# Optimization experiments

Measured on AMD Instinct MI355X. Metric: run time of the kernel, lower is better.

## Reference

```python
import jax, jax.numpy as jnp
import numpy as np

N = 10000        # nodes
E = 160000       # active edges
NS = 128         # scalar (0e) channels per tensor
NV = 64          # vector (1o) channels per tensor
LAT = 64         # latent dim
AVG_NEIGH = 16.0
SQ2 = float(np.sqrt(2.0))
SQ3 = float(np.sqrt(3.0))
EPS = 1e-5


def setup_inputs() -> dict:
    key = jax.random.key(0)
    ks = jax.random.split(key, 24)
    rn = lambda k, s: jax.random.normal(k, s, jnp.float32)
    d = {}
    d["latents"] = rn(ks[0], (E, LAT))
    d["node_features"] = rn(ks[1], (N, NS + 3 * NV))
    d["edge_features"] = rn(ks[2], (E, NS + 3 * NV))
    d["edge_sh"] = rn(ks[3], (E, 4))
    d["edge_index"] = jax.random.randint(ks[4], (2, E), 0, N)
    d["atom_type"] = jax.random.randint(ks[5], (N,), 0, 10)
    d["active_edges"] = jnp.arange(E)
    # separable layer norm affine params (node and edge)
    d["g_s_n"] = jnp.ones((NS,), jnp.float32); d["b_s_n"] = jnp.zeros((NS,), jnp.float32)
    d["g_v_n"] = jnp.ones((NV,), jnp.float32)
    d["g_s_e"] = jnp.ones((NS,), jnp.float32); d["b_s_e"] = jnp.zeros((NS,), jnp.float32)
    d["g_v_e"] = jnp.ones((NV,), jnp.float32)
    # FullyConnectedTensorProduct weights (path-normalized init).
    # tp input: 2*NS scalars, 2*NV vectors; sh: 1 scalar + 1 vector;
    # tp output: NS+NV scalars (scalars+gates), NV vectors.
    nSt, nVt, nSo = 2 * NS, 2 * NV, NS + NV
    d["W_ss0"] = rn(ks[6], (nSt, nSo)) / np.sqrt(nSt * 2)
    d["W_vv0"] = rn(ks[7], (nVt, nSo)) / np.sqrt(nVt * 2)
    d["W_sv1"] = rn(ks[8], (nSt, NV)) / np.sqrt(nSt * 3)
    d["W_vs1"] = rn(ks[9], (nVt, NV)) / np.sqrt(nVt * 3)
    d["W_vv1"] = rn(ks[10], (nVt, NV)) / np.sqrt(nVt * 3)
    # lin_post (per-l channel mixing)
    d["Wp_s"] = rn(ks[11], (NS, NS)) / np.sqrt(NS)
    d["Wp_v"] = rn(ks[12], (NV, NV)) / np.sqrt(NV)
    # env_embed_mlps: single linear latent -> weight_numel (NS+NV channels)
    d["W_env"] = rn(ks[13], (LAT, NS + NV)) / np.sqrt(LAT)
    # linear_res
    d["Wr_s"] = rn(ks[14], (NS, NS)) / np.sqrt(NS)
    d["Wr_v"] = rn(ks[15], (NV, NV)) / np.sqrt(NV)
    return d


def _sep_ln(x, g_s, b_s, g_v):
    # separable layer norm: standard LN on scalars, RMS-of-norms on vectors
    s = x[:, :NS]
    v = x[:, NS:].reshape(-1, NV, 3)
    mu = s.mean(-1, keepdims=True)
    var = ((s - mu) ** 2).mean(-1, keepdims=True)
    s = (s - mu) * jax.lax.rsqrt(var + EPS) * g_s + b_s
    vn = jnp.mean(jnp.sum(v * v, -1), -1, keepdims=True)  # (B,1)
    v = v * jax.lax.rsqrt(vn + EPS)[:, :, None] * g_v[None, :, None]
    return s, v


def _forward(latents, node_features, edge_features, edge_sh, edge_index,
             atom_type, active_edges,
             g_s_n, b_s_n, g_v_n, g_s_e, b_s_e, g_v_e,
             W_ss0, W_vv0, W_sv1, W_vs1, W_vv1,
             Wp_s, Wp_v, W_env, Wr_s, Wr_v):
    ec = edge_index[0][active_edges]                      # (E,) center nodes
    ns, nv = _sep_ln(node_features, g_s_n, b_s_n, g_v_n)
    es, ev = _sep_ln(edge_features, g_s_e, b_s_e, g_v_e)
    S = jnp.concatenate([ns[ec], es], axis=-1)            # (E, 2*NS)
    V = jnp.concatenate([nv[ec], ev], axis=1)             # (E, 2*NV, 3)
    sh0 = edge_sh[:, :1]                                  # (E,1)
    sh1 = edge_sh[:, 1:]                                  # (E,3)
    # fully-connected tensor product (tp_in x sh -> gate input)
    dotV = jnp.einsum('ecd,ed->ec', V, sh1) / SQ3         # 1x1->0
    out0 = (S * sh0) @ W_ss0 + dotV @ W_vv0               # (E, NS+NV) scalars
    out_v = (S @ W_sv1)[:, :, None] * sh1[:, None, :]     # 0x1->1
    out_v = out_v + jnp.einsum('ecd,cf->efd', V, W_vs1) * sh0[:, :, None]  # 1x0->1
    cross = jnp.cross(V, sh1[:, None, :]) / SQ2           # 1x1->1
    out_v = out_v + jnp.einsum('ecd,cf->efd', cross, W_vv1)  # (E, NV, 3)
    # gate
    s = jax.nn.silu(out0[:, :NS])
    gates = jax.nn.sigmoid(out0[:, NS:])
    v = out_v * gates[:, :, None]
    # lin_post
    s = s @ Wp_s
    v = jnp.einsum('ecd,cf->efd', v, Wp_v)
    # env weights from latents (elementwise linear per channel)
    w = latents[active_edges] @ W_env                     # (E, NS+NV)
    s = s * w[:, :NS]
    v = v * w[:, NS:][:, :, None]
    msg = jnp.concatenate([s, v.reshape(-1, 3 * NV)], axis=-1)  # (E, 320)
    agg = jax.ops.segment_sum(msg, ec, num_segments=N)
    agg = agg * jnp.float32(1.0 / np.sqrt(AVG_NEIGH))
    # residual linear on raw node features
    rs = node_features[:, :NS] @ Wr_s
    rv = jnp.einsum('ncd,cf->nfd', node_features[:, NS:].reshape(-1, NV, 3), Wr_v)
    res = jnp.concatenate([rs, rv.reshape(-1, 3 * NV)], axis=-1)
    return res + agg


def reference(latents, node_features, edge_features, edge_sh, edge_index,
              atom_type, active_edges,
              g_s_n, b_s_n, g_v_n, g_s_e, b_s_e, g_v_e,
              W_ss0, W_vv0, W_sv1, W_vs1, W_vv1,
              Wp_s, Wp_v, W_env, Wr_s, Wr_v):
    return _forward(latents, node_features, edge_features, edge_sh, edge_index,
                    atom_type, active_edges,
                    g_s_n, b_s_n, g_v_n, g_s_e, b_s_e, g_v_e,
                    W_ss0, W_vv0, W_sv1, W_vs1, W_vv1,
                    Wp_s, Wp_v, W_env, Wr_s, Wr_v)
```

## Files before the change

kernel.cpp:

```cpp
#include <hip/hip_runtime.h>

#define N_NODES 10000
#define N_EDGES 160000
#define NSC 128
#define ROW 320
#define EPS_LN 1e-5f
#define INV_SQ2 0.70710678118654752440f
#define INV_SQ3 0.57735026918962576451f

typedef unsigned short bfraw;
typedef __attribute__((ext_vector_type(8))) short short8;
typedef __attribute__((ext_vector_type(4))) float float4x;

__device__ __forceinline__ float bf2f(bfraw u) {
    union { unsigned int i; float f; } x; x.i = ((unsigned int)u) << 16; return x.f;
}
__device__ __forceinline__ bfraw f2bf(float f) {
    union { float f; unsigned int i; } x; x.f = f;
    unsigned int i = x.i;
    unsigned int lsb = (i >> 16) & 1u;
    i += 0x7fffu + lsb;
    return (bfraw)(i >> 16);
}
template<bool B> __device__ __forceinline__ float LD(const void* p, size_t i) {
    if (B) return bf2f(((const bfraw*)p)[i]);
    else   return ((const float*)p)[i];
}
template<bool B> __device__ __forceinline__ void ST(void* p, size_t i, float v) {
    if (B) ((bfraw*)p)[i] = f2bf(v);
    else   ((float*)p)[i] = v;
}
__device__ __forceinline__ float wred64(float v) {
#pragma unroll
    for (int o = 32; o > 0; o >>= 1) v += __shfl_xor(v, o, 64);
    return v;
}
__device__ __forceinline__ void wredx12(float a[12]) {
#pragma unroll
    for (int o = 32; o > 0; o >>= 1) {
        float t[12];
#pragma unroll
        for (int i = 0; i < 12; i++) t[i] = __shfl_xor(a[i], o, 64);
#pragma unroll
        for (int i = 0; i < 12; i++) a[i] += t[i];
    }
}
__device__ __forceinline__ float silu_f(float x) { return x / (1.0f + __expf(-x)); }
__device__ __forceinline__ float sigm_f(float x) { return 1.0f / (1.0f + __expf(-x)); }

#define MFMA16(a, b, c) __builtin_amdgcn_mfma_f32_16x16x32_bf16((a), (b), (c), 0, 0, 0)

__device__ __forceinline__ int SDI(int r, int c) { return r * 384 + (c ^ ((r & 7) << 3)); }
__device__ __forceinline__ int X64(int r, int c) { return r * 64  + (c ^ ((r & 7) << 3)); }
__device__ __forceinline__ int SPI(int r, int c) { return r * 128 + (c ^ ((r & 7) << 3)); }
__device__ __forceinline__ int WVI(int r, int c) { return r * 192 + (c ^ ((r & 7) << 2)); }

__global__ void detect_k(const void* g, int* flag) {
    if (threadIdx.x == 0 && blockIdx.x == 0)
        *flag = (((const unsigned int*)g)[0] == 0x3F803F80u) ? 1 : 0;
}

__global__ void pack_all_k(
    const void* Wss0, const void* Wvv0, const void* Wsv1, const void* Wvs1,
    const void* Wvv1, const void* Wps,  const void* Wpv,  const void* Wenv,
    const void* Wrs,  const void* Wrv,
    bfraw* __restrict__ dst, const int* __restrict__ flag)
{
    int idx = blockIdx.x * 256 + threadIdx.x;
    if (idx >= 159744) return;
    const void* src; int K, N, base;
    if      (idx <  49152) { src = Wss0; K = 256; N = 192; base = 0; }
    else if (idx <  73728) { src = Wvv0; K = 128; N = 192; base = 49152; }
    else if (idx <  90112) { src = Wsv1; K = 256; N =  64; base = 73728; }
    else if (idx <  98304) { src = Wvs1; K = 128; N =  64; base = 90112; }
    else if (idx < 106496) { src = Wvv1; K = 128; N =  64; base = 98304; }
    else if (idx < 122880) { src = Wps;  K = 128; N = 128; base = 106496; }
    else if (idx < 126976) { src = Wpv;  K =  64; N =  64; base = 122880; }
    else if (idx < 139264) { src = Wenv; K =  64; N = 192; base = 126976; }
    else if (idx < 155648) { src = Wrs;  K = 128; N = 128; base = 139264; }
    else                   { src = Wrv;  K =  64; N =  64; base = 155648; }
    int li = idx - base;
    int j = li & 7, l = (li >> 3) & 63, t = li >> 9;
    int NT = N >> 4;
    int nt = t % NT, kt = t / NT;
    int k = kt * 32 + ((l >> 4) << 3) + j;
    int n = (nt << 4) + (l & 15);
    float v = (*flag) ? bf2f(((const bfraw*)src)[(size_t)k * N + n])
                      : ((const float*)src)[(size_t)k * N + n];
    dst[idx] = f2bf(v);
}

__global__ void count_k(const int* __restrict__ eidx, const int* __restrict__ act,
                        int* __restrict__ counts) {
    int e = blockIdx.x * 256 + threadIdx.x;
    if (e < N_EDGES) atomicAdd(&counts[eidx[act[e]]], 1);
}

__global__ __launch_bounds__(1024) void scan_k(const int* __restrict__ counts,
                                               int* __restrict__ starts) {
    __shared__ int wsum[16];
    int t = threadIdx.x;
    int lo = t * 10;
    int lanev = t & 63, wv = t >> 6;
    int c[10];
    int s = 0;
    if (lo < N_NODES) {
#pragma unroll
        for (int j = 0; j < 10; j++) { c[j] = counts[lo + j]; s += c[j]; }
    }
    int ps = s;
#pragma unroll
    for (int o = 1; o < 64; o <<= 1) {
        int u = __shfl_up(ps, o, 64);
        if (lanev >= o) ps += u;
    }
    if (lanev == 63) wsum[wv] = ps;
    __syncthreads();
    if (t == 0) {
        int acc = 0;
#pragma unroll
        for (int i = 0; i < 16; i++) { int v = wsum[i]; wsum[i] = acc; acc += v; }
        starts[N_NODES] = acc;
    }
    __syncthreads();
    if (lo < N_NODES) {
        int acc = wsum[wv] + ps - s;
#pragma unroll
        for (int j = 0; j < 10; j++) { starts[lo + j] = acc; acc += c[j]; }
    }
}

__global__ void fill_k(const int* __restrict__ eidx, const int* __restrict__ act,
                       const int* __restrict__ starts, int* __restrict__ cursor,
                       int* __restrict__ csr) {
    int e = blockIdx.x * 256 + threadIdx.x;
    if (e < N_EDGES) {
        int n = eidx[act[e]];
        int pos = atomicAdd(&cursor[n], 1);
        csr[starts[n] + pos] = e;
    }
}

template<bool B>
__device__ __forceinline__ void node_ln_body(int n, int lane,
    const void* nf, const void* g_s, const void* b_s, const void* g_v,
    float* __restrict__ nsnv)
{
    size_t base = (size_t)n * ROW;
    float s0 = LD<B>(nf, base + lane), s1 = LD<B>(nf, base + 64 + lane);
    float mu = wred64(s0 + s1) * (1.0f / 128.0f);
    float d0 = s0 - mu, d1 = s1 - mu;
    float var = wred64(d0 * d0 + d1 * d1) * (1.0f / 128.0f);
    float rs = rsqrtf(var + EPS_LN);
    float o0 = d0 * rs * LD<B>(g_s, lane) + LD<B>(b_s, lane);
    float o1 = d1 * rs * LD<B>(g_s, 64 + lane) + LD<B>(b_s, 64 + lane);
    float vx = LD<B>(nf, base + NSC + 3 * lane);
    float vy = LD<B>(nf, base + NSC + 3 * lane + 1);
    float vz = LD<B>(nf, base + NSC + 3 * lane + 2);
    float vn = wred64(vx * vx + vy * vy + vz * vz) * (1.0f / 64.0f);
    float rv = rsqrtf(vn + EPS_LN) * LD<B>(g_v, lane);
    float* o = nsnv + base;
    o[lane] = o0; o[64 + lane] = o1;
    o[NSC + 3 * lane] = vx * rv; o[NSC + 3 * lane + 1] = vy * rv; o[NSC + 3 * lane + 2] = vz * rv;
}

__global__ __launch_bounds__(256) void node_ln_k(
    const void* nf, const void* g_s, const void* b_s, const void* g_v,
    float* __restrict__ nsnv, const int* __restrict__ flag)
{
    int w = threadIdx.x >> 6, lane = threadIdx.x & 63;
    int n = blockIdx.x * 4 + w;
    if (*flag) node_ln_body<true >(n, lane, nf, g_s, b_s, g_v, nsnv);
    else       node_ln_body<false>(n, lane, nf, g_s, b_s, g_v, nsnv);
}

template<bool B>
__device__ void edge_body(char* smem, int tid,
    const float* __restrict__ nsnv,
    const void* ef, const void* esh,
    const int* __restrict__ eidx, const int* __restrict__ act,
    const void* lat,
    const void* g_s_e, const void* b_s_e, const void* g_v_e,
    const bfraw* __restrict__ pk,
    bfraw* __restrict__ msg)
{
    bfraw* SD     = (bfraw*)(smem);
    bfraw* Vn     = (bfraw*)(smem + 12288);
    bfraw* Ve     = (bfraw*)(smem + 18432);
    bfraw* gate_u = (bfraw*)(smem + 18432);
    bfraw* sp_u   = (bfraw*)(smem + 20480);
    bfraw* lat_u  = (bfraw*)(smem + 24576);
    float* sh_f   = (float*)(smem + 26624);
    float* wenv_f = (float*)(smem);

    const bfraw* pWss0 = pk;
    const bfraw* pWvv0 = pk + 49152;
    const bfraw* pWsv1 = pk + 73728;
    const bfraw* pWvs1 = pk + 90112;
    const bfraw* pWvv1 = pk + 98304;
    const bfraw* pWps  = pk + 106496;
    const bfraw* pWpv  = pk + 122880;
    const bfraw* pWenv = pk + 126976;

    const int w = tid >> 6, lane = tid & 63;
    const int nl = lane & 15, mq = lane >> 4;
    const int e0 = blockIdx.x * 16;

    float gse0 = LD<B>(g_s_e, lane), gse1 = LD<B>(g_s_e, 64 + lane);
    float bse0 = LD<B>(b_s_e, lane), bse1 = LD<B>(b_s_e, 64 + lane);
    float gve  = LD<B>(g_v_e, lane);

    float es0[4], es1[4], ex[4], ey[4], ez[4];
    float shv[4][4];
#pragma unroll
    for (int i = 0; i < 4; i++) {
        int el = w * 4 + i, e = e0 + el;
        int ae = act[e];
        int cnv = eidx[ae];
        shv[i][0] = LD<B>(esh, (size_t)e * 4 + 0);
        shv[i][1] = LD<B>(esh, (size_t)e * 4 + 1);
        shv[i][2] = LD<B>(esh, (size_t)e * 4 + 2);
        shv[i][3] = LD<B>(esh, (size_t)e * 4 + 3);
        size_t eb = (size_t)e * ROW;
        es0[i] = LD<B>(ef, eb + lane);
        es1[i] = LD<B>(ef, eb + 64 + lane);
        ex[i]  = LD<B>(ef, eb + NSC + 3 * lane);
        ey[i]  = LD<B>(ef, eb + NSC + 3 * lane + 1);
        ez[i]  = LD<B>(ef, eb + NSC + 3 * lane + 2);
        float la = LD<B>(lat, (size_t)ae * 64 + lane);
        const float* nr = nsnv + (size_t)cnv * ROW;
        float n0 = nr[lane], n1 = nr[64 + lane];
        float nx = nr[NSC + 3 * lane], ny = nr[NSC + 3 * lane + 1], nz = nr[NSC + 3 * lane + 2];
        SD[SDI(el, lane)]       = f2bf(n0);
        SD[SDI(el, 64 + lane)]  = f2bf(n1);
        SD[SDI(el, 256 + lane)] = f2bf((nx * shv[i][1] + ny * shv[i][2] + nz * shv[i][3]) * INV_SQ3);
        Vn[X64(el, lane)]       = f2bf(nx);
        Vn[X64(16 + el, lane)]  = f2bf(ny);
        Vn[X64(32 + el, lane)]  = f2bf(nz);
        lat_u[X64(el, lane)]    = f2bf(la);
        if (lane == 0) {
            sh_f[el * 4]     = shv[i][0]; sh_f[el * 4 + 1] = shv[i][1];
            sh_f[el * 4 + 2] = shv[i][2]; sh_f[el * 4 + 3] = shv[i][3];
        }
    }
    float red[12];
#pragma unroll
    for (int i = 0; i < 4; i++) {
        red[i]     = es0[i] + es1[i];
        red[4 + i] = es0[i] * es0[i] + es1[i] * es1[i];
        red[8 + i] = ex[i] * ex[i] + ey[i] * ey[i] + ez[i] * ez[i];
    }
    wredx12(red);
#pragma unroll
    for (int i = 0; i < 4; i++) {
        int el = w * 4 + i;
        float mu  = red[i] * (1.0f / 128.0f);
        float var = red[4 + i] * (1.0f / 128.0f) - mu * mu;
        float rs  = rsqrtf(var + EPS_LN);
        float o0  = (es0[i] - mu) * rs * gse0 + bse0;
        float o1  = (es1[i] - mu) * rs * gse1 + bse1;
        float rv  = rsqrtf(red[8 + i] * (1.0f / 64.0f) + EPS_LN) * gve;
        float exn = ex[i] * rv, eyn = ey[i] * rv, ezn = ez[i] * rv;
        SD[SDI(el, 128 + lane)] = f2bf(o0);
        SD[SDI(el, 192 + lane)] = f2bf(o1);
        SD[SDI(el, 320 + lane)] = f2bf((exn * shv[i][1] + eyn * shv[i][2] + ezn * shv[i][3]) * INV_SQ3);
        Ve[X64(el, lane)]       = f2bf(exn);
        Ve[X64(16 + el, lane)]  = f2bf(eyn);
        Ve[X64(32 + el, lane)]  = f2bf(ezn);
    }
    __syncthreads();

    float o_g1[3][4];
    {
        float4x sA[3] = {{0,0,0,0},{0,0,0,0},{0,0,0,0}};
        float4x dA[3] = {{0,0,0,0},{0,0,0,0},{0,0,0,0}};
#pragma unroll
        for (int kt = 0; kt < 8; kt++) {
            short8 a = *(const short8*)&SD[SDI(nl, kt * 32 + mq * 8)];
#pragma unroll
            for (int t = 0; t < 3; t++) {
                short8 b = *(const short8*)&pWss0[((kt * 12 + 3 * w + t) * 64 + lane) * 8];
                sA[t] = MFMA16(a, b, sA[t]);
            }
        }
#pragma unroll
        for (int kt = 0; kt < 4; kt++) {
            short8 a = *(const short8*)&SD[SDI(nl, 256 + kt * 32 + mq * 8)];
#pragma unroll
            for (int t = 0; t < 3; t++) {
                short8 b = *(const short8*)&pWvv0[((kt * 12 + 3 * w + t) * 64 + lane) * 8];
                dA[t] = MFMA16(a, b, dA[t]);
            }
        }
#pragma unroll
        for (int t = 0; t < 3; t++)
#pragma unroll
            for (int r = 0; r < 4; r++)
                o_g1[t][r] = sh_f[(mq * 4 + r) * 4] * sA[t][r] + dA[t][r];
    }
    float sv[4];
    {
        float4x c = {0,0,0,0};
#pragma unroll
        for (int kt = 0; kt < 8; kt++) {
            short8 a = *(const short8*)&SD[SDI(nl, kt * 32 + mq * 8)];
            short8 b = *(const short8*)&pWsv1[((kt * 4 + w) * 64 + lane) * 8];
            c = MFMA16(a, b, c);
        }
#pragma unroll
        for (int r = 0; r < 4; r++) sv[r] = c[r];
    }
    float4x H[3] = {{0,0,0,0},{0,0,0,0},{0,0,0,0}};
    float4x K[3] = {{0,0,0,0},{0,0,0,0},{0,0,0,0}};
#pragma unroll
    for (int d = 0; d < 3; d++) {
#pragma unroll
        for (int kt = 0; kt < 4; kt++) {
            short8 a = (kt < 2)
                ? *(const short8*)&Vn[X64(d * 16 + nl, kt * 32 + mq * 8)]
                : *(const short8*)&Ve[X64(d * 16 + nl, (kt - 2) * 32 + mq * 8)];
            short8 bH = *(const short8*)&pWvs1[((kt * 4 + w) * 64 + lane) * 8];
            short8 bK = *(const short8*)&pWvv1[((kt * 4 + w) * 64 + lane) * 8];
            H[d] = MFMA16(a, bH, H[d]);
            K[d] = MFMA16(a, bK, K[d]);
        }
    }
    __syncthreads();

#pragma unroll
    for (int t = 0; t < 3; t++) {
        int tile = 3 * w + t;
#pragma unroll
        for (int r = 0; r < 4; r++) {
            int el = mq * 4 + r;
            float o = o_g1[t][r];
            if (tile < 8) sp_u[SPI(el, tile * 16 + nl)]         = f2bf(silu_f(o));
            else          gate_u[X64(el, (tile - 8) * 16 + nl)] = f2bf(sigm_f(o));
        }
    }
    __syncthreads();

    {
        int f = w * 16 + nl;
#pragma unroll
        for (int r = 0; r < 4; r++) {
            int el = mq * 4 + r;
            float g   = bf2f(gate_u[X64(el, f)]);
            float svv = sv[r];
            float s0v = sh_f[el * 4], b0 = sh_f[el * 4 + 1], b1 = sh_f[el * 4 + 2], b2 = sh_f[el * 4 + 3];
            float ov0 = svv * b0 + s0v * H[0][r] + (b2 * K[1][r] - b1 * K[2][r]) * INV_SQ2;
            float ov1 = svv * b1 + s0v * H[1][r] + (b0 * K[2][r] - b2 * K[0][r]) * INV_SQ2;
            float ov2 = svv * b2 + s0v * H[2][r] + (b1 * K[0][r] - b0 * K[1][r]) * INV_SQ2;
            Vn[X64(el, f)]      = f2bf(ov0 * g);
            Vn[X64(16 + el, f)] = f2bf(ov1 * g);
            Vn[X64(32 + el, f)] = f2bf(ov2 * g);
        }
    }
    __syncthreads();

    float4x s2[2] = {{0,0,0,0},{0,0,0,0}};
#pragma unroll
    for (int kt = 0; kt < 4; kt++) {
        short8 a = *(const short8*)&sp_u[SPI(nl, kt * 32 + mq * 8)];
#pragma unroll
        for (int t = 0; t < 2; t++) {
            short8 b = *(const short8*)&pWps[((kt * 8 + w + 4 * t) * 64 + lane) * 8];
            s2[t] = MFMA16(a, b, s2[t]);
        }
    }
    float4x v2[3] = {{0,0,0,0},{0,0,0,0},{0,0,0,0}};
#pragma unroll
    for (int d = 0; d < 3; d++) {
#pragma unroll
        for (int kt = 0; kt < 2; kt++) {
            short8 a = *(const short8*)&Vn[X64(d * 16 + nl, kt * 32 + mq * 8)];
            short8 b = *(const short8*)&pWpv[((kt * 4 + w) * 64 + lane) * 8];
            v2[d] = MFMA16(a, b, v2[d]);
        }
    }
    float4x wv[3] = {{0,0,0,0},{0,0,0,0},{0,0,0,0}};
#pragma unroll
    for (int kt = 0; kt < 2; kt++) {
        short8 a = *(const short8*)&lat_u[X64(nl, kt * 32 + mq * 8)];
#pragma unroll
        for (int t = 0; t < 3; t++) {
            short8 b = *(const short8*)&pWenv[((kt * 12 + 3 * w + t) * 64 + lane) * 8];
            wv[t] = MFMA16(a, b, wv[t]);
        }
    }
#pragma unroll
    for (int t = 0; t < 3; t++)
#pragma unroll
        for (int r = 0; r < 4; r++)
            wenv_f[WVI(mq * 4 + r, (3 * w + t) * 16 + nl)] = wv[t][r];
    __syncthreads();

#pragma unroll
    for (int t = 0; t < 2; t++) {
        int c = (w + 4 * t) * 16 + nl;
#pragma unroll
        for (int r = 0; r < 4; r++) {
            int el = mq * 4 + r;
            msg[(size_t)(e0 + el) * 320 + c] = f2bf(s2[t][r] * wenv_f[WVI(el, c)]);
        }
    }
    {
        int f = w * 16 + nl;
#pragma unroll
        for (int r = 0; r < 4; r++) {
            int el = mq * 4 + r;
            float we = wenv_f[WVI(el, 128 + f)];
            size_t base = (size_t)(e0 + el) * 320 + NSC + 3 * f;
            msg[base]     = f2bf(v2[0][r] * we);
            msg[base + 1] = f2bf(v2[1][r] * we);
            msg[base + 2] = f2bf(v2[2][r] * we);
        }
    }
}

__global__ __launch_bounds__(256, 5) void edge_mfma_k(
    const float* __restrict__ nsnv,
    const void* ef, const void* esh,
    const int* __restrict__ eidx, const int* __restrict__ act,
    const void* lat,
    const void* g_s_e, const void* b_s_e, const void* g_v_e,
    const bfraw* __restrict__ pk,
    bfraw* __restrict__ msg, const int* __restrict__ flag)
{
    __shared__ __align__(16) char smem[26880];
    if (*flag) edge_body<true >(smem, threadIdx.x, nsnv, ef, esh, eidx, act, lat,
        g_s_e, b_s_e, g_v_e, pk, msg);
    else       edge_body<false>(smem, threadIdx.x, nsnv, ef, esh, eidx, act, lat,
        g_s_e, b_s_e, g_v_e, pk, msg);
}

__global__ __launch_bounds__(256) void gather_k(
    const bfraw* __restrict__ msg, const int* __restrict__ starts,
    const int* __restrict__ csr, float* __restrict__ agg)
{
    int w = threadIdx.x >> 6, lane = threadIdx.x & 63;
    int n = blockIdx.x * 4 + w;
    if (n >= N_NODES) return;
    int s0 = starts[n], s1 = starts[n + 1];
    float a0 = 0, a1 = 0, a2 = 0, a3 = 0, a4 = 0;
    int i = s0;
    for (; i + 1 < s1; i += 2) {
        const bfraw* r0 = msg + (size_t)csr[i] * 320;
        const bfraw* r1 = msg + (size_t)csr[i + 1] * 320;
        a0 += bf2f(r0[lane])       + bf2f(r1[lane]);
        a1 += bf2f(r0[64 + lane])  + bf2f(r1[64 + lane]);
        a2 += bf2f(r0[128 + lane]) + bf2f(r1[128 + lane]);
        a3 += bf2f(r0[192 + lane]) + bf2f(r1[192 + lane]);
        a4 += bf2f(r0[256 + lane]) + bf2f(r1[256 + lane]);
    }
    if (i < s1) {
        const bfraw* r = msg + (size_t)csr[i] * 320;
        a0 += bf2f(r[lane]);
        a1 += bf2f(r[64 + lane]);
        a2 += bf2f(r[128 + lane]);
        a3 += bf2f(r[192 + lane]);
        a4 += bf2f(r[256 + lane]);
    }
    float* o = agg + (size_t)n * ROW;
    o[lane] = a0; o[64 + lane] = a1; o[128 + lane] = a2; o[192 + lane] = a3; o[256 + lane] = a4;
}

template<bool B>
__device__ void final_body(char* smem, int tid,
    const void* nf, const float* __restrict__ agg,
    const bfraw* __restrict__ pk, void* out)
{
    bfraw* Sn_u = (bfraw*)(smem);
    bfraw* Vn_u = (bfraw*)(smem + 8704);
    const bfraw* pWrs = pk + 139264;
    const bfraw* pWrv = pk + 155648;

    const int w = tid >> 6, lane = tid & 63;
    const int nl = lane & 15, mq = lane >> 4;
    const int n0b = blockIdx.x * 32;

    for (int i = 0; i < 8; i++) {
        int el = w * 8 + i;
        int n = n0b + el;
        bool ok = n < N_NODES;
        size_t base = (size_t)n * ROW;
        float a0 = ok ? LD<B>(nf, base + lane) : 0.0f;
        float a1 = ok ? LD<B>(nf, base + 64 + lane) : 0.0f;
        float vx = ok ? LD<B>(nf, base + NSC + 3 * lane) : 0.0f;
        float vy = ok ? LD<B>(nf, base + NSC + 3 * lane + 1) : 0.0f;
        float vz = ok ? LD<B>(nf, base + NSC + 3 * lane + 2) : 0.0f;
        Sn_u[el * 136 + lane]      = f2bf(a0);
        Sn_u[el * 136 + 64 + lane] = f2bf(a1);
        Vn_u[(el) * 72 + lane]      = f2bf(vx);
        Vn_u[(32 + el) * 72 + lane] = f2bf(vy);
        Vn_u[(64 + el) * 72 + lane] = f2bf(vz);
    }
    __syncthreads();

    {
        const int mt = w & 1, ntb = (w >> 1) * 4;
        float4x c[4] = {{0,0,0,0},{0,0,0,0},{0,0,0,0},{0,0,0,0}};
#pragma unroll
        for (int kt = 0; kt < 4; kt++) {
            short8 a = *(const short8*)&Sn_u[(mt * 16 + nl) * 136 + kt * 32 + mq * 8];
#pragma unroll
            for (int t = 0; t < 4; t++) {
                short8 b = *(const short8*)&pWrs[((kt * 8 + ntb + t) * 64 + lane) * 8];
                c[t] = MFMA16(a, b, c[t]);
            }
        }
#pragma unroll
        for (int t = 0; t < 4; t++) {
            int cc = (ntb + t) * 16 + nl;
#pragma unroll
            for (int r = 0; r < 4; r++) {
                int n = n0b + mt * 16 + mq * 4 + r;
                if (n < N_NODES) {
                    size_t o = (size_t)n * ROW + cc;
                    ST<B>(out, o, c[t][r] + 0.25f * agg[o]);
                }
            }
        }
    }
    {
        float4x c[3][2] = {{{0,0,0,0},{0,0,0,0}},{{0,0,0,0},{0,0,0,0}},{{0,0,0,0},{0,0,0,0}}};
#pragma unroll
        for (int d = 0; d < 3; d++)
#pragma unroll
            for (int h = 0; h < 2; h++)
#pragma unroll
                for (int kt = 0; kt < 2; kt++) {
                    short8 a = *(const short8*)&Vn_u[(d * 32 + h * 16 + nl) * 72 + kt * 32 + mq * 8];
                    short8 b = *(const short8*)&pWrv[((kt * 4 + w) * 64 + lane) * 8];
                    c[d][h] = MFMA16(a, b, c[d][h]);
                }
        int f = w * 16 + nl;
#pragma unroll
        for (int h = 0; h < 2; h++)
#pragma unroll
            for (int r = 0; r < 4; r++) {
                int n = n0b + h * 16 + mq * 4 + r;
                if (n < N_NODES) {
                    size_t o = (size_t)n * ROW + NSC + 3 * f;
                    ST<B>(out, o,     c[0][h][r] + 0.25f * agg[o]);
                    ST<B>(out, o + 1, c[1][h][r] + 0.25f * agg[o + 1]);
                    ST<B>(out, o + 2, c[2][h][r] + 0.25f * agg[o + 2]);
                }
            }
    }
}

__global__ __launch_bounds__(256) void final_mfma_k(
    const void* nf, const float* __restrict__ agg,
    const bfraw* __restrict__ pk, void* out, const int* __restrict__ flag)
{
    __shared__ __align__(16) char smem[22528];
    if (*flag) final_body<true >(smem, threadIdx.x, nf, agg, pk, out);
    else       final_body<false>(smem, threadIdx.x, nf, agg, pk, out);
}

extern "C" void kernel_launch(void* const* d_in, const int* in_sizes, int n_in,
                              void* d_out, int out_size, void* d_ws, size_t ws_size,
                              hipStream_t stream)
{
    const void* latents = d_in[0];
    const void* node_f  = d_in[1];
    const void* edge_f  = d_in[2];
    const void* edge_sh = d_in[3];
    const int* edge_index = (const int*)d_in[4];
    const int* active     = (const int*)d_in[6];
    const void* g_s_n = d_in[7];
    const void* b_s_n = d_in[8];
    const void* g_v_n = d_in[9];
    const void* g_s_e = d_in[10];
    const void* b_s_e = d_in[11];
    const void* g_v_e = d_in[12];

    char* ws = (char*)d_ws;
    int*   flag   = (int*)ws;
    float* agg    = (float*)(ws + 256);
    float* nsnv   = (float*)(ws + 12800256);
    bfraw* pk     = (bfraw*)(ws + 25600256);
    int*   counts = (int*)(ws + 25919744);
    int*   cursor = (int*)(ws + 25960704);
    int*   starts = (int*)(ws + 26001664);
    int*   csr    = (int*)(ws + 26042624);
    bfraw* msg    = (bfraw*)(ws + 26682624);

    detect_k<<<1, 64, 0, stream>>>(g_s_n, flag);
    hipMemsetAsync(counts, 0, 81920, stream);
    pack_all_k<<<624, 256, 0, stream>>>(d_in[13], d_in[14], d_in[15], d_in[16],
        d_in[17], d_in[18], d_in[19], d_in[20], d_in[21], d_in[22], pk, flag);
    count_k<<<625, 256, 0, stream>>>(edge_index, active, counts);
    scan_k<<<1, 1024, 0, stream>>>(counts, starts);
    fill_k<<<625, 256, 0, stream>>>(edge_index, active, starts, cursor, csr);
    node_ln_k<<<N_NODES / 4, 256, 0, stream>>>(node_f, g_s_n, b_s_n, g_v_n, nsnv, flag);
    edge_mfma_k<<<N_EDGES / 16, 256, 0, stream>>>(nsnv, edge_f, edge_sh, edge_index, active,
        latents, g_s_e, b_s_e, g_v_e, pk, msg, flag);
    gather_k<<<N_NODES / 4, 256, 0, stream>>>(msg, starts, csr, agg);
    final_mfma_k<<<(N_NODES + 31) / 32, 256, 0, stream>>>(node_f, agg, pk, (void*)d_out, flag);
}
```

Baseline: 596.1 us.

## Fuse prep kernels, double-buffer MFMA weight loads, vectorize gather

Folds weight packing, degree counting and node layer norm into one prep kernel, and computes the dtype flag inline so the detect kernel and two launches go away. In the edge kernel, weight fragments are loaded from global memory two k-steps ahead and the scalar-to-vector product is fused into the first GEMM loop. Launch bounds drop from 5 to 4 waves to make room for the extra registers. The gather kernel now reads two bf16 values per 32-bit load and writes float2 pairs. Trade-offs are lower occupancy and more register pressure in the edge kernel.

```diff
diff --git a/kernel.cpp b/kernel.cpp
--- a/kernel.cpp
+++ b/kernel.cpp
@@ -11,6 +11,7 @@
 typedef unsigned short bfraw;
 typedef __attribute__((ext_vector_type(8))) short short8;
 typedef __attribute__((ext_vector_type(4))) float float4x;
+typedef __attribute__((ext_vector_type(2))) float float2x;
 
 __device__ __forceinline__ float bf2f(bfraw u) {
     union { unsigned int i; float f; } x; x.i = ((unsigned int)u) << 16; return x.f;
@@ -55,19 +56,15 @@
 __device__ __forceinline__ int SPI(int r, int c) { return r * 128 + (c ^ ((r & 7) << 3)); }
 __device__ __forceinline__ int WVI(int r, int c) { return r * 192 + (c ^ ((r & 7) << 2)); }
 
-__global__ void detect_k(const void* g, int* flag) {
-    if (threadIdx.x == 0 && blockIdx.x == 0)
-        *flag = (((const unsigned int*)g)[0] == 0x3F803F80u) ? 1 : 0;
-}
-
-__global__ void pack_all_k(
+__device__ __forceinline__ int dtype_flag(const void* g_s_n) {
+    return (((const unsigned int*)g_s_n)[0] == 0x3F803F80u) ? 1 : 0;
+}
+
+__device__ __forceinline__ void pack_body(int idx, int fl,
     const void* Wss0, const void* Wvv0, const void* Wsv1, const void* Wvs1,
     const void* Wvv1, const void* Wps,  const void* Wpv,  const void* Wenv,
-    const void* Wrs,  const void* Wrv,
-    bfraw* __restrict__ dst, const int* __restrict__ flag)
-{
-    int idx = blockIdx.x * 256 + threadIdx.x;
-    if (idx >= 159744) return;
+    const void* Wrs,  const void* Wrv,  bfraw* __restrict__ dst)
+{
     const void* src; int K, N, base;
     if      (idx <  49152) { src = Wss0; K = 256; N = 192; base = 0; }
     else if (idx <  73728) { src = Wvv0; K = 128; N = 192; base = 49152; }
@@ -85,60 +82,9 @@
     int nt = t % NT, kt = t / NT;
     int k = kt * 32 + ((l >> 4) << 3) + j;
     int n = (nt << 4) + (l & 15);
-    float v = (*flag) ? bf2f(((const bfraw*)src)[(size_t)k * N + n])
-                      : ((const float*)src)[(size_t)k * N + n];
+    float v = fl ? bf2f(((const bfraw*)src)[(size_t)k * N + n])
+                 : ((const float*)src)[(size_t)k * N + n];
     dst[idx] = f2bf(v);
-}
-
-__global__ void count_k(const int* __restrict__ eidx, const int* __restrict__ act,
-                        int* __restrict__ counts) {
-    int e = blockIdx.x * 256 + threadIdx.x;
-    if (e < N_EDGES) atomicAdd(&counts[eidx[act[e]]], 1);
-}
-
-__global__ __launch_bounds__(1024) void scan_k(const int* __restrict__ counts,
-                                               int* __restrict__ starts) {
-    __shared__ int wsum[16];
-    int t = threadIdx.x;
-    int lo = t * 10;
-    int lanev = t & 63, wv = t >> 6;
-    int c[10];
-    int s = 0;
-    if (lo < N_NODES) {
-#pragma unroll
-        for (int j = 0; j < 10; j++) { c[j] = counts[lo + j]; s += c[j]; }
-    }
-    int ps = s;
-#pragma unroll
-    for (int o = 1; o < 64; o <<= 1) {
-        int u = __shfl_up(ps, o, 64);
-        if (lanev >= o) ps += u;
-    }
-    if (lanev == 63) wsum[wv] = ps;
-    __syncthreads();
-    if (t == 0) {
-        int acc = 0;
-#pragma unroll
-        for (int i = 0; i < 16; i++) { int v = wsum[i]; wsum[i] = acc; acc += v; }
-        starts[N_NODES] = acc;
-    }
-    __syncthreads();
-    if (lo < N_NODES) {
-        int acc = wsum[wv] + ps - s;
-#pragma unroll
-        for (int j = 0; j < 10; j++) { starts[lo + j] = acc; acc += c[j]; }
-    }
-}
-
-__global__ void fill_k(const int* __restrict__ eidx, const int* __restrict__ act,
-                       const int* __restrict__ starts, int* __restrict__ cursor,
-                       int* __restrict__ csr) {
-    int e = blockIdx.x * 256 + threadIdx.x;
-    if (e < N_EDGES) {
-        int n = eidx[act[e]];
-        int pos = atomicAdd(&cursor[n], 1);
-        csr[starts[n] + pos] = e;
-    }
 }
 
 template<bool B>
@@ -164,14 +110,69 @@
     o[NSC + 3 * lane] = vx * rv; o[NSC + 3 * lane + 1] = vy * rv; o[NSC + 3 * lane + 2] = vz * rv;
 }
 
-__global__ __launch_bounds__(256) void node_ln_k(
-    const void* nf, const void* g_s, const void* b_s, const void* g_v,
-    float* __restrict__ nsnv, const int* __restrict__ flag)
-{
+__global__ __launch_bounds__(256) void prep_k(
+    const void* Wss0, const void* Wvv0, const void* Wsv1, const void* Wvs1,
+    const void* Wvv1, const void* Wps,  const void* Wpv,  const void* Wenv,
+    const void* Wrs,  const void* Wrv,  bfraw* __restrict__ pk,
+    const int* __restrict__ eidx, const int* __restrict__ act, int* __restrict__ counts,
+    const void* nf, const void* g_s_n, const void* b_s_n, const void* g_v_n,
+    float* __restrict__ nsnv)
+{
+    int fl = dtype_flag(g_s_n);
+    int idx = blockIdx.x * 256 + threadIdx.x;
+    if (idx < 159744)
+        pack_body(idx, fl, Wss0, Wvv0, Wsv1, Wvs1, Wvv1, Wps, Wpv, Wenv, Wrs, Wrv, pk);
+    if (idx < N_EDGES)
+        atomicAdd(&counts[eidx[act[idx]]], 1);
     int w = threadIdx.x >> 6, lane = threadIdx.x & 63;
     int n = blockIdx.x * 4 + w;
-    if (*flag) node_ln_body<true >(n, lane, nf, g_s, b_s, g_v, nsnv);
-    else       node_ln_body<false>(n, lane, nf, g_s, b_s, g_v, nsnv);
+    if (fl) node_ln_body<true >(n, lane, nf, g_s_n, b_s_n, g_v_n, nsnv);
+    else    node_ln_body<false>(n, lane, nf, g_s_n, b_s_n, g_v_n, nsnv);
+}
+
+__global__ __launch_bounds__(1024) void scan_k(const int* __restrict__ counts,
+                                               int* __restrict__ starts) {
+    __shared__ int wsum[16];
+    int t = threadIdx.x;
+    int lo = t * 10;
+    int lanev = t & 63, wv = t >> 6;
+    int c[10];
+    int s = 0;
+    if (lo < N_NODES) {
+#pragma unroll
+        for (int j = 0; j < 10; j++) { c[j] = counts[lo + j]; s += c[j]; }
+    }
+    int ps = s;
+#pragma unroll
+    for (int o = 1; o < 64; o <<= 1) {
+        int u = __shfl_up(ps, o, 64);
+        if (lanev >= o) ps += u;
+    }
+    if (lanev == 63) wsum[wv] = ps;
+    __syncthreads();
+    if (t == 0) {
+        int acc = 0;
+#pragma unroll
+        for (int i = 0; i < 16; i++) { int v = wsum[i]; wsum[i] = acc; acc += v; }
+        starts[N_NODES] = acc;
+    }
+    __syncthreads();
+    if (lo < N_NODES) {
+        int acc = wsum[wv] + ps - s;
+#pragma unroll
+        for (int j = 0; j < 10; j++) { starts[lo + j] = acc; acc += c[j]; }
+    }
+}
+
+__global__ void fill_k(const int* __restrict__ eidx, const int* __restrict__ act,
+                       const int* __restrict__ starts, int* __restrict__ cursor,
+                       int* __restrict__ csr) {
+    int e = blockIdx.x * 256 + threadIdx.x;
+    if (e < N_EDGES) {
+        int n = eidx[act[e]];
+        int pos = atomicAdd(&cursor[n], 1);
+        csr[starts[n] + pos] = e;
+    }
 }
 
 template<bool B>
@@ -210,13 +211,17 @@
     float bse0 = LD<B>(b_s_e, lane), bse1 = LD<B>(b_s_e, 64 + lane);
     float gve  = LD<B>(g_v_e, lane);
 
+    int ae_[4], cn_[4];
+#pragma unroll
+    for (int i = 0; i < 4; i++) ae_[i] = act[e0 + w * 4 + i];
+#pragma unroll
+    for (int i = 0; i < 4; i++) cn_[i] = eidx[ae_[i]];
+
     float es0[4], es1[4], ex[4], ey[4], ez[4];
     float shv[4][4];
 #pragma unroll
     for (int i = 0; i < 4; i++) {
         int el = w * 4 + i, e = e0 + el;
-        int ae = act[e];
-        int cnv = eidx[ae];
         shv[i][0] = LD<B>(esh, (size_t)e * 4 + 0);
         shv[i][1] = LD<B>(esh, (size_t)e * 4 + 1);
         shv[i][2] = LD<B>(esh, (size_t)e * 4 + 2);
@@ -227,8 +232,8 @@
         ex[i]  = LD<B>(ef, eb + NSC + 3 * lane);
         ey[i]  = LD<B>(ef, eb + NSC + 3 * lane + 1);
         ez[i]  = LD<B>(ef, eb + NSC + 3 * lane + 2);
-        float la = LD<B>(lat, (size_t)ae * 64 + lane);
-        const float* nr = nsnv + (size_t)cnv * ROW;
+        float la = LD<B>(lat, (size_t)ae_[i] * 64 + lane);
+        const float* nr = nsnv + (size_t)cn_[i] * ROW;
         float n0 = nr[lane], n1 = nr[64 + lane];
         float nx = nr[NSC + 3 * lane], ny = nr[NSC + 3 * lane + 1], nz = nr[NSC + 3 * lane + 2];
         SD[SDI(el, lane)]       = f2bf(n0);
@@ -270,59 +275,85 @@
     }
     __syncthreads();
 
-    float o_g1[3][4];
-    {
-        float4x sA[3] = {{0,0,0,0},{0,0,0,0},{0,0,0,0}};
-        float4x dA[3] = {{0,0,0,0},{0,0,0,0},{0,0,0,0}};
+    float4x sA0={0,0,0,0}, sA1={0,0,0,0}, sA2={0,0,0,0}, cSV={0,0,0,0};
+    {
+        const bfraw* ps = pWss0 + (size_t)(3 * w * 64 + lane) * 8;
+        const bfraw* pv = pWsv1 + (size_t)(w * 64 + lane) * 8;
+        short8 b0[4], b1[4];
+#define LDG1(kt, D) do { \
+        D[0] = *(const short8*)(ps + (kt) * 6144);        \
+        D[1] = *(const short8*)(ps + (kt) * 6144 + 512);  \
+        D[2] = *(const short8*)(ps + (kt) * 6144 + 1024); \
+        D[3] = *(const short8*)(pv + (kt) * 2048); } while (0)
+        LDG1(0, b0); LDG1(1, b1);
 #pragma unroll
         for (int kt = 0; kt < 8; kt++) {
             short8 a = *(const short8*)&SD[SDI(nl, kt * 32 + mq * 8)];
-#pragma unroll
-            for (int t = 0; t < 3; t++) {
-                short8 b = *(const short8*)&pWss0[((kt * 12 + 3 * w + t) * 64 + lane) * 8];
-                sA[t] = MFMA16(a, b, sA[t]);
+            if ((kt & 1) == 0) {
+                sA0 = MFMA16(a, b0[0], sA0); sA1 = MFMA16(a, b0[1], sA1);
+                sA2 = MFMA16(a, b0[2], sA2); cSV = MFMA16(a, b0[3], cSV);
+                if (kt + 2 < 8) LDG1(kt + 2, b0);
+            } else {
+                sA0 = MFMA16(a, b1[0], sA0); sA1 = MFMA16(a, b1[1], sA1);
+                sA2 = MFMA16(a, b1[2], sA2); cSV = MFMA16(a, b1[3], cSV);
+                if (kt + 2 < 8) LDG1(kt + 2, b1);
             }
         }
+#undef LDG1
+    }
+    float4x dA0={0,0,0,0}, dA1={0,0,0,0}, dA2={0,0,0,0};
+    {
+        const bfraw* pd = pWvv0 + (size_t)(3 * w * 64 + lane) * 8;
+        short8 c0[3], c1[3];
+#define LDGD(kt, D) do { \
+        D[0] = *(const short8*)(pd + (kt) * 6144);        \
+        D[1] = *(const short8*)(pd + (kt) * 6144 + 512);  \
+        D[2] = *(const short8*)(pd + (kt) * 6144 + 1024); } while (0)
+        LDGD(0, c0); LDGD(1, c1);
 #pragma unroll
         for (int kt = 0; kt < 4; kt++) {
             short8 a = *(const short8*)&SD[SDI(nl, 256 + kt * 32 + mq * 8)];
-#pragma unroll
-            for (int t = 0; t < 3; t++) {
-                short8 b = *(const short8*)&pWvv0[((kt * 12 + 3 * w + t) * 64 + lane) * 8];
-                dA[t] = MFMA16(a, b, dA[t]);
+            if ((kt & 1) == 0) {
+                dA0 = MFMA16(a, c0[0], dA0); dA1 = MFMA16(a, c0[1], dA1); dA2 = MFMA16(a, c0[2], dA2);
+                if (kt + 2 < 4) LDGD(kt + 2, c0);
+            } else {
+                dA0 = MFMA16(a, c1[0], dA0); dA1 = MFMA16(a, c1[1], dA1); dA2 = MFMA16(a, c1[2], dA2);
+                if (kt + 2 < 4) LDGD(kt + 2, c1);
             }
         }
-#pragma unroll
-        for (int t = 0; t < 3; t++)
-#pragma unroll
-            for (int r = 0; r < 4; r++)
-                o_g1[t][r] = sh_f[(mq * 4 + r) * 4] * sA[t][r] + dA[t][r];
-    }
-    float sv[4];
-    {
-        float4x c = {0,0,0,0};
-#pragma unroll
-        for (int kt = 0; kt < 8; kt++) {
-            short8 a = *(const short8*)&SD[SDI(nl, kt * 32 + mq * 8)];
-            short8 b = *(const short8*)&pWsv1[((kt * 4 + w) * 64 + lane) * 8];
-            c = MFMA16(a, b, c);
-        }
-#pragma unroll
-        for (int r = 0; r < 4; r++) sv[r] = c[r];
+#undef LDGD
+    }
+    float o_g1[3][4];
+#pragma unroll
+    for (int r = 0; r < 4; r++) {
+        float sh0 = sh_f[(mq * 4 + r) * 4];
+        o_g1[0][r] = sh0 * sA0[r] + dA0[r];
+        o_g1[1][r] = sh0 * sA1[r] + dA1[r];
+        o_g1[2][r] = sh0 * sA2[r] + dA2[r];
     }
     float4x H[3] = {{0,0,0,0},{0,0,0,0},{0,0,0,0}};
     float4x K[3] = {{0,0,0,0},{0,0,0,0},{0,0,0,0}};
-#pragma unroll
-    for (int d = 0; d < 3; d++) {
-#pragma unroll
-        for (int kt = 0; kt < 4; kt++) {
-            short8 a = (kt < 2)
-                ? *(const short8*)&Vn[X64(d * 16 + nl, kt * 32 + mq * 8)]
-                : *(const short8*)&Ve[X64(d * 16 + nl, (kt - 2) * 32 + mq * 8)];
-            short8 bH = *(const short8*)&pWvs1[((kt * 4 + w) * 64 + lane) * 8];
-            short8 bK = *(const short8*)&pWvv1[((kt * 4 + w) * 64 + lane) * 8];
-            H[d] = MFMA16(a, bH, H[d]);
-            K[d] = MFMA16(a, bK, K[d]);
+    {
+        const bfraw* ph = pWvs1 + (size_t)(w * 64 + lane) * 8;
+        const bfraw* pq = pWvv1 + (size_t)(w * 64 + lane) * 8;
+        short8 gH0 = *(const short8*)(ph);
+        short8 gH1 = *(const short8*)(ph + 2048);
+        short8 gH2 = *(const short8*)(ph + 4096);
+        short8 gH3 = *(const short8*)(ph + 6144);
+        short8 gK0 = *(const short8*)(pq);
+        short8 gK1 = *(const short8*)(pq + 2048);
+        short8 gK2 = *(const short8*)(pq + 4096);
+        short8 gK3 = *(const short8*)(pq + 6144);
+#pragma unroll
+        for (int d = 0; d < 3; d++) {
+            short8 a0 = *(const short8*)&Vn[X64(d * 16 + nl, mq * 8)];
+            short8 a1 = *(const short8*)&Vn[X64(d * 16 + nl, 32 + mq * 8)];
+            short8 a2 = *(const short8*)&Ve[X64(d * 16 + nl, mq * 8)];
+            short8 a3 = *(const short8*)&Ve[X64(d * 16 + nl, 32 + mq * 8)];
+            H[d] = MFMA16(a0, gH0, H[d]); K[d] = MFMA16(a0, gK0, K[d]);
+            H[d] = MFMA16(a1, gH1, H[d]); K[d] = MFMA16(a1, gK1, K[d]);
+            H[d] = MFMA16(a2, gH2, H[d]); K[d] = MFMA16(a2, gK2, K[d]);
+            H[d] = MFMA16(a3, gH3, H[d]); K[d] = MFMA16(a3, gK3, K[d]);
         }
     }
     __syncthreads();
@@ -346,7 +377,7 @@
         for (int r = 0; r < 4; r++) {
             int el = mq * 4 + r;
             float g   = bf2f(gate_u[X64(el, f)]);
-            float svv = sv[r];
+            float svv = cSV[r];
             float s0v = sh_f[el * 4], b0 = sh_f[el * 4 + 1], b1 = sh_f[el * 4 + 2], b2 = sh_f[el * 4 + 3];
             float ov0 = svv * b0 + s0v * H[0][r] + (b2 * K[1][r] - b1 * K[2][r]) * INV_SQ2;
             float ov1 = svv * b1 + s0v * H[1][r] + (b0 * K[2][r] - b2 * K[0][r]) * INV_SQ2;
@@ -358,50 +389,73 @@
     }
     __syncthreads();
 
-    float4x s2[2] = {{0,0,0,0},{0,0,0,0}};
-#pragma unroll
-    for (int kt = 0; kt < 4; kt++) {
-        short8 a = *(const short8*)&sp_u[SPI(nl, kt * 32 + mq * 8)];
-#pragma unroll
-        for (int t = 0; t < 2; t++) {
-            short8 b = *(const short8*)&pWps[((kt * 8 + w + 4 * t) * 64 + lane) * 8];
-            s2[t] = MFMA16(a, b, s2[t]);
-        }
+    float4x s2_0 = {0,0,0,0}, s2_1 = {0,0,0,0};
+    {
+        const bfraw* pp = pWps + (size_t)(w * 64 + lane) * 8;
+        short8 u0[2], u1[2];
+#define LDS2(kt, D) do { \
+        D[0] = *(const short8*)(pp + (kt) * 4096);         \
+        D[1] = *(const short8*)(pp + (kt) * 4096 + 2048); } while (0)
+        LDS2(0, u0); LDS2(1, u1);
+#pragma unroll
+        for (int kt = 0; kt < 4; kt++) {
+            short8 a = *(const short8*)&sp_u[SPI(nl, kt * 32 + mq * 8)];
+            if ((kt & 1) == 0) {
+                s2_0 = MFMA16(a, u0[0], s2_0); s2_1 = MFMA16(a, u0[1], s2_1);
+                if (kt + 2 < 4) LDS2(kt + 2, u0);
+            } else {
+                s2_0 = MFMA16(a, u1[0], s2_0); s2_1 = MFMA16(a, u1[1], s2_1);
+                if (kt + 2 < 4) LDS2(kt + 2, u1);
+            }
+        }
+#undef LDS2
+    }
+    float4x wv0 = {0,0,0,0}, wv1 = {0,0,0,0}, wv2 = {0,0,0,0};
+    {
+        const bfraw* pe = pWenv + (size_t)(3 * w * 64 + lane) * 8;
+        short8 e00 = *(const short8*)(pe);
+        short8 e01 = *(const short8*)(pe + 512);
+        short8 e02 = *(const short8*)(pe + 1024);
+        short8 e10 = *(const short8*)(pe + 6144);
+        short8 e11 = *(const short8*)(pe + 6144 + 512);
+        short8 e12 = *(const short8*)(pe + 6144 + 1024);
+        short8 a0 = *(const short8*)&lat_u[X64(nl, mq * 8)];
+        short8 a1 = *(const short8*)&lat_u[X64(nl, 32 + mq * 8)];
+        wv0 = MFMA16(a0, e00, wv0); wv0 = MFMA16(a1, e10, wv0);
+        wv1 = MFMA16(a0, e01, wv1); wv1 = MFMA16(a1, e11, wv1);
+        wv2 = MFMA16(a0, e02, wv2); wv2 = MFMA16(a1, e12, wv2);
     }
     float4x v2[3] = {{0,0,0,0},{0,0,0,0},{0,0,0,0}};
-#pragma unroll
-    for (int d = 0; d < 3; d++) {
-#pragma unroll
-        for (int kt = 0; kt < 2; kt++) {
-            short8 a = *(const short8*)&Vn[X64(d * 16 + nl, kt * 32 + mq * 8)];
-            short8 b = *(const short8*)&pWpv[((kt * 4 + w) * 64 + lane) * 8];
-            v2[d] = MFMA16(a, b, v2[d]);
-        }
-    }
-    float4x wv[3] = {{0,0,0,0},{0,0,0,0},{0,0,0,0}};
-#pragma unroll
-    for (int kt = 0; kt < 2; kt++) {
-        short8 a = *(const short8*)&lat_u[X64(nl, kt * 32 + mq * 8)];
-#pragma unroll
-        for (int t = 0; t < 3; t++) {
-            short8 b = *(const short8*)&pWenv[((kt * 12 + 3 * w + t) * 64 + lane) * 8];
-            wv[t] = MFMA16(a, b, wv[t]);
-        }
-    }
-#pragma unroll
-    for (int t = 0; t < 3; t++)
-#pragma unroll
-        for (int r = 0; r < 4; r++)
-            wenv_f[WVI(mq * 4 + r, (3 * w + t) * 16 + nl)] = wv[t][r];
+    {
+        const bfraw* pz = pWpv + (size_t)(w * 64 + lane) * 8;
+        short8 z0 = *(const short8*)(pz);
+        short8 z1 = *(const short8*)(pz + 2048);
+#pragma unroll
+        for (int d = 0; d < 3; d++) {
+            short8 a0 = *(const short8*)&Vn[X64(d * 16 + nl, mq * 8)];
+            short8 a1 = *(const short8*)&Vn[X64(d * 16 + nl, 32 + mq * 8)];
+            v2[d] = MFMA16(a0, z0, v2[d]);
+            v2[d] = MFMA16(a1, z1, v2[d]);
+        }
+    }
+    {
+        float4x wvv[3] = {wv0, wv1, wv2};
+#pragma unroll
+        for (int t = 0; t < 3; t++)
+#pragma unroll
+            for (int r = 0; r < 4; r++)
+                wenv_f[WVI(mq * 4 + r, (3 * w + t) * 16 + nl)] = wvv[t][r];
+    }
     __syncthreads();
 
 #pragma unroll
     for (int t = 0; t < 2; t++) {
         int c = (w + 4 * t) * 16 + nl;
+        float4x s2v = (t == 0) ? s2_0 : s2_1;
 #pragma unroll
         for (int r = 0; r < 4; r++) {
             int el = mq * 4 + r;
-            msg[(size_t)(e0 + el) * 320 + c] = f2bf(s2[t][r] * wenv_f[WVI(el, c)]);
+            msg[(size_t)(e0 + el) * 320 + c] = f2bf(s2v[r] * wenv_f[WVI(el, c)]);
         }
     }
     {
@@ -418,21 +472,26 @@
     }
 }
 
-__global__ __launch_bounds__(256, 5) void edge_mfma_k(
+__global__ __launch_bounds__(256, 4) void edge_mfma_k(
     const float* __restrict__ nsnv,
     const void* ef, const void* esh,
     const int* __restrict__ eidx, const int* __restrict__ act,
     const void* lat,
     const void* g_s_e, const void* b_s_e, const void* g_v_e,
     const bfraw* __restrict__ pk,
-    bfraw* __restrict__ msg, const int* __restrict__ flag)
+    bfraw* __restrict__ msg, const void* g_s_n)
 {
     __shared__ __align__(16) char smem[26880];
-    if (*flag) edge_body<true >(smem, threadIdx.x, nsnv, ef, esh, eidx, act, lat,
-        g_s_e, b_s_e, g_v_e, pk, msg);
-    else       edge_body<false>(smem, threadIdx.x, nsnv, ef, esh, eidx, act, lat,
-        g_s_e, b_s_e, g_v_e, pk, msg);
-}
+    if (dtype_flag(g_s_n))
+        edge_body<true >(smem, threadIdx.x, nsnv, ef, esh, eidx, act, lat,
+                         g_s_e, b_s_e, g_v_e, pk, msg);
+    else
+        edge_body<false>(smem, threadIdx.x, nsnv, ef, esh, eidx, act, lat,
+                         g_s_e, b_s_e, g_v_e, pk, msg);
+}
+
+__device__ __forceinline__ float lo16(unsigned u) { return bf2f((bfraw)(u & 0xffffu)); }
+__device__ __forceinline__ float hi16(unsigned u) { return bf2f((bfraw)(u >> 16)); }
 
 __global__ __launch_bounds__(256) void gather_k(
     const bfraw* __restrict__ msg, const int* __restrict__ starts,
@@ -442,27 +501,33 @@
     int n = blockIdx.x * 4 + w;
     if (n >= N_NODES) return;
     int s0 = starts[n], s1 = starts[n + 1];
-    float a0 = 0, a1 = 0, a2 = 0, a3 = 0, a4 = 0;
+    bool half = lane < 32;
+    float l0 = 0, h0 = 0, l1 = 0, h1 = 0, l2 = 0, h2 = 0;
     int i = s0;
     for (; i + 1 < s1; i += 2) {
-        const bfraw* r0 = msg + (size_t)csr[i] * 320;
-        const bfraw* r1 = msg + (size_t)csr[i + 1] * 320;
-        a0 += bf2f(r0[lane])       + bf2f(r1[lane]);
-        a1 += bf2f(r0[64 + lane])  + bf2f(r1[64 + lane]);
-        a2 += bf2f(r0[128 + lane]) + bf2f(r1[128 + lane]);
-        a3 += bf2f(r0[192 + lane]) + bf2f(r1[192 + lane]);
-        a4 += bf2f(r0[256 + lane]) + bf2f(r1[256 + lane]);
+        const unsigned* r0 = (const unsigned*)(msg + (size_t)csr[i] * 320);
+        const unsigned* r1 = (const unsigned*)(msg + (size_t)csr[i + 1] * 320);
+        unsigned a00 = r0[lane], a01 = r0[64 + lane];
+        unsigned a10 = r1[lane], a11 = r1[64 + lane];
+        unsigned a02 = half ? r0[128 + lane] : 0u;
+        unsigned a12 = half ? r1[128 + lane] : 0u;
+        l0 += lo16(a00) + lo16(a10); h0 += hi16(a00) + hi16(a10);
+        l1 += lo16(a01) + lo16(a11); h1 += hi16(a01) + hi16(a11);
+        l2 += lo16(a02) + lo16(a12); h2 += hi16(a02) + hi16(a12);
     }
     if (i < s1) {
-        const bfraw* r = msg + (size_t)csr[i] * 320;
-        a0 += bf2f(r[lane]);
-        a1 += bf2f(r[64 + lane]);
-        a2 += bf2f(r[128 + lane]);
-        a3 += bf2f(r[192 + lane]);
-        a4 += bf2f(r[256 + lane]);
+        const unsigned* r = (const unsigned*)(msg + (size_t)csr[i] * 320);
+        unsigned a0 = r[lane], a1 = r[64 + lane];
+        unsigned a2 = half ? r[128 + lane] : 0u;
+        l0 += lo16(a0); h0 += hi16(a0);
+        l1 += lo16(a1); h1 += hi16(a1);
+        l2 += lo16(a2); h2 += hi16(a2);
     }
     float* o = agg + (size_t)n * ROW;
-    o[lane] = a0; o[64 + lane] = a1; o[128 + lane] = a2; o[192 + lane] = a3; o[256 + lane] = a4;
+    float2x v0 = {l0, h0}, v1 = {l1, h1}, v2 = {l2, h2};
+    ((float2x*)o)[lane] = v0;
+    ((float2x*)(o + 128))[lane] = v1;
+    if (half) ((float2x*)(o + 256))[lane] = v2;
 }
 
 template<bool B>
@@ -552,11 +617,11 @@
 
 __global__ __launch_bounds__(256) void final_mfma_k(
     const void* nf, const float* __restrict__ agg,
-    const bfraw* __restrict__ pk, void* out, const int* __restrict__ flag)
+    const bfraw* __restrict__ pk, void* out, const void* g_s_n)
 {
     __shared__ __align__(16) char smem[22528];
-    if (*flag) final_body<true >(smem, threadIdx.x, nf, agg, pk, out);
-    else       final_body<false>(smem, threadIdx.x, nf, agg, pk, out);
+    if (dtype_flag(g_s_n)) final_body<true >(smem, threadIdx.x, nf, agg, pk, out);
+    else                   final_body<false>(smem, threadIdx.x, nf, agg, pk, out);
 }
 
 extern "C" void kernel_launch(void* const* d_in, const int* in_sizes, int n_in,
@@ -577,7 +642,6 @@
     const void* g_v_e = d_in[12];
 
     char* ws = (char*)d_ws;
-    int*   flag   = (int*)ws;
     float* agg    = (float*)(ws + 256);
     float* nsnv   = (float*)(ws + 12800256);
     bfraw* pk     = (bfraw*)(ws + 25600256);
@@ -587,16 +651,14 @@
     int*   csr    = (int*)(ws + 26042624);
     bfraw* msg    = (bfraw*)(ws + 26682624);
 
-    detect_k<<<1, 64, 0, stream>>>(g_s_n, flag);
     hipMemsetAsync(counts, 0, 81920, stream);
-    pack_all_k<<<624, 256, 0, stream>>>(d_in[13], d_in[14], d_in[15], d_in[16],
-        d_in[17], d_in[18], d_in[19], d_in[20], d_in[21], d_in[22], pk, flag);
-    count_k<<<625, 256, 0, stream>>>(edge_index, active, counts);
+    prep_k<<<2500, 256, 0, stream>>>(d_in[13], d_in[14], d_in[15], d_in[16],
+        d_in[17], d_in[18], d_in[19], d_in[20], d_in[21], d_in[22], pk,
+        edge_index, active, counts, node_f, g_s_n, b_s_n, g_v_n, nsnv);
     scan_k<<<1, 1024, 0, stream>>>(counts, starts);
     fill_k<<<625, 256, 0, stream>>>(edge_index, active, starts, cursor, csr);
-    node_ln_k<<<N_NODES / 4, 256, 0, stream>>>(node_f, g_s_n, b_s_n, g_v_n, nsnv, flag);
     edge_mfma_k<<<N_EDGES / 16, 256, 0, stream>>>(nsnv, edge_f, edge_sh, edge_index, active,
-        latents, g_s_e, b_s_e, g_v_e, pk, msg, flag);
+        latents, g_s_e, b_s_e, g_v_e, pk, msg, g_s_n);
     gather_k<<<N_NODES / 4, 256, 0, stream>>>(msg, starts, csr, agg);
-    final_mfma_k<<<(N_NODES + 31) / 32, 256, 0, stream>>>(node_f, agg, pk, (void*)d_out, flag);
-}
+    final_mfma_k<<<(N_NODES + 31) / 32, 256, 0, stream>>>(node_f, agg, pk, (void*)d_out, g_s_n);
+}
```

After: 581.4 us. 2.5% less time.
